# Performance work log

Hardware: AMD Instinct MI355X
Metric: run time of the kernel (lower is better)

## Reference

```python
import jax, jax.numpy as jnp
import numpy as np

N_QUBITS = 4
N_LAYERS = 2
DIM = 2 ** N_QUBITS  # 16
B = 65536


def _apply_1q(state, U, wire):
    # state: (B,) + (2,)*N_QUBITS complex64; U: (2,2) complex. Wire 0 = most significant (PennyLane order).
    s = jnp.moveaxis(state, wire + 1, -1)
    s = jnp.einsum('...j,ij->...i', s, U)
    return jnp.moveaxis(s, -1, wire + 1)


def _apply_cnot(state, control, target):
    s = jnp.moveaxis(state, (control + 1, target + 1), (-2, -1))
    s = jnp.concatenate([s[..., 0:1, :], s[..., 1:2, ::-1]], axis=-2)
    return jnp.moveaxis(s, (-2, -1), (control + 1, target + 1))


def _rot_matrix(phi, th, om):
    # qml.Rot(phi, theta, omega) = RZ(om) RY(th) RZ(phi)
    c = jnp.cos(th / 2)
    sn = jnp.sin(th / 2)
    ep = jnp.exp(-0.5j * (phi + om).astype(jnp.complex64))
    em = jnp.exp(0.5j * (phi - om).astype(jnp.complex64))
    row0 = jnp.stack([ep * c, -em * sn])
    row1 = jnp.stack([jnp.conj(em) * sn, jnp.conj(ep) * c])
    return jnp.stack([row0, row1])


def _strongly_entangling(state, theta):
    # PennyLane StronglyEntanglingLayers, default ranges r_l = (l % (n-1)) + 1, CNOT imprimitive ring
    for l in range(N_LAYERS):
        for w in range(N_QUBITS):
            U = _rot_matrix(theta[l, w, 0], theta[l, w, 1], theta[l, w, 2])
            state = _apply_1q(state, U, w)
        r = (l % (N_QUBITS - 1)) + 1
        for w in range(N_QUBITS):
            state = _apply_cnot(state, w, (w + r) % N_QUBITS)
    return state


def _encode(x, W1, b1, W2, b2):
    v = x.reshape(x.shape[0], -1) @ W1 + b1
    v = jax.nn.relu(v)
    v = v @ W2 + b2
    v = jnp.nan_to_num(v, nan=0.0, posinf=1.0, neginf=-1.0)
    v = jnp.tanh(v)
    nrm = jnp.linalg.norm(v, axis=-1, keepdims=True)
    return v / jnp.maximum(nrm, 1e-8)  # F.normalize(p=2, eps=1e-8)


def _prepare_state(v, theta):
    # AmplitudeEmbedding(normalize=True): renormalize, embed as amplitudes
    v = v / jnp.linalg.norm(v, axis=-1, keepdims=True)
    state = v.astype(jnp.complex64).reshape((v.shape[0],) + (2,) * N_QUBITS)
    return _strongly_entangling(state, theta)


def setup_inputs() -> dict:
    key = jax.random.key(0)
    k = jax.random.split(key, 7)
    return {
        'img_a': jax.random.normal(k[0], (B, 1, 28, 28), dtype=jnp.float32),
        'img_b': jax.random.normal(k[1], (B, 1, 28, 28), dtype=jnp.float32),
        'W1': 0.05 * jax.random.normal(k[2], (784, 64), dtype=jnp.float32),
        'b1': 0.05 * jax.random.normal(k[3], (64,), dtype=jnp.float32),
        'W2': 0.05 * jax.random.normal(k[4], (64, 16), dtype=jnp.float32),
        'b2': 0.05 * jax.random.normal(k[5], (16,), dtype=jnp.float32),
        'theta': 0.05 * jax.random.normal(k[6], (N_LAYERS, N_QUBITS, 3), dtype=jnp.float32),
    }


def reference(img_a, img_b, W1, b1, W2, b2, theta):
    theta_safe = jnp.nan_to_num(theta, nan=0.0, posinf=1.0, neginf=-1.0)
    va = _encode(img_a, W1, b1, W2, b2)
    vb = _encode(img_b, W1, b1, W2, b2)
    sa = _prepare_state(va, theta_safe).reshape(-1, DIM)
    sb = _prepare_state(vb, theta_safe).reshape(-1, DIM)
    # SWAP test: p0 = (1 + |<a|b>|^2)/2  =>  clamp(2*p0 - 1, 0, 1) = clip(|<a|b>|^2, 0, 1)
    ov = jnp.einsum('bd,bd->b', jnp.conj(sa), sb)
    fid = jnp.clip(jnp.abs(ov) ** 2, 0.0, 1.0)
    return fid.astype(jnp.float32)
```

## Files before the change

### kernel.cpp

```cpp
#include <hip/hip_runtime.h>


#define KDIM   784
#define HDIM   64
#define KSTEPS 25
#define W1S_ELEMS (KSTEPS * 4 * 64 * 8)
#define W1S_BYTES (W1S_ELEMS * 2)

typedef float  f32x4  __attribute__((ext_vector_type(4)));
typedef short  bf16x8 __attribute__((ext_vector_type(8)));

__device__ __forceinline__ unsigned short f2bf(float f) {
  unsigned u = __float_as_uint(f);
  u += 0x7fffu + ((u >> 16) & 1u);
  return (unsigned short)(u >> 16);
}

__device__ __forceinline__ float bf2f(unsigned short h) {
  return __uint_as_float(((unsigned)h) << 16);
}

__device__ __forceinline__ bf16x8 cvt8(f32x4 lo, f32x4 hi) {
  bf16x8 r;
  r[0] = (short)f2bf(lo[0]); r[1] = (short)f2bf(lo[1]);
  r[2] = (short)f2bf(lo[2]); r[3] = (short)f2bf(lo[3]);
  r[4] = (short)f2bf(hi[0]); r[5] = (short)f2bf(hi[1]);
  r[6] = (short)f2bf(hi[2]); r[7] = (short)f2bf(hi[3]);
  return r;
}

__device__ __forceinline__ float tanh_fast(float x) {
  float e = __expf(2.0f * x);
  return 1.0f - 2.0f / (e + 1.0f);
}

__global__ __launch_bounds__(256)
void prep_kernel(const float* __restrict__ W1, const float* __restrict__ W2,
                 unsigned short* __restrict__ w1s, float* __restrict__ w2t) {
  int tid = blockIdx.x * 256 + threadIdx.x;
  if (tid < W1S_ELEMS) {
    int j  = tid & 7;
    int l  = (tid >> 3) & 63;
    int st = tid >> 9;
    int s  = st >> 2;
    int t  = st & 3;
    int k  = s * 32 + (l >> 4) * 8 + j;
    int n  = t * 16 + (l & 15);
    float v = (k < KDIM) ? W1[k * HDIM + n] : 0.0f;
    w1s[tid] = f2bf(v);
  }
  if (tid < HDIM * 16) {
    int c = tid >> 6;
    int k = tid & 63;
    w2t[c * HDIM + k] = W2[k * 16 + c];
  }
}

__global__ __launch_bounds__(256, 8)
void qcm_kernel(const float* __restrict__ img_a, const float* __restrict__ img_b,
                const float* __restrict__ b1,    const float* __restrict__ b2,
                const unsigned short* __restrict__ w1s,
                const float* __restrict__ w2t,
                float* __restrict__ out) {
  __shared__ __attribute__((aligned(16))) unsigned short lds_h[64][72];

  const int tid  = threadIdx.x;
  const int wave = tid >> 6;
  const int lane = tid & 63;
  const int m    = lane & 15;
  const int quad = lane >> 4;
  const int p0   = blockIdx.x * 32 + wave * 8;

  const float* row = (m < 8)
      ? (img_a + (size_t)(p0 + m)     * KDIM)
      : (img_b + (size_t)(p0 + m - 8) * KDIM);
  const int koff = quad * 8;

  f32x4 acc[4];
  #pragma unroll
  for (int t = 0; t < 4; ++t)
    acc[t][0] = acc[t][1] = acc[t][2] = acc[t][3] = 0.0f;

  const int4* bwl = (const int4*)w1s + lane;
  f32x4 z4; z4[0] = z4[1] = z4[2] = z4[3] = 0.0f;

  f32x4 c0 = *(const f32x4*)(row + koff);
  f32x4 c1 = *(const f32x4*)(row + koff + 4);

  for (int s = 0; s < KSTEPS; ++s) {
    int4 w0 = bwl[s * 256];
    int4 w1 = bwl[s * 256 + 64];
    int4 w2 = bwl[s * 256 + 128];
    int4 w3 = bwl[s * 256 + 192];

    f32x4 n0 = z4, n1 = z4;
    if (s < 23) {
      const int kb = (s + 1) * 32 + koff;
      n0 = *(const f32x4*)(row + kb);
      n1 = *(const f32x4*)(row + kb + 4);
    } else if (s == 23) {
      if (quad < 2) {
        n0 = *(const f32x4*)(row + 768 + koff);
        n1 = *(const f32x4*)(row + 768 + koff + 4);
      }
    }

    bf16x8 fa = cvt8(c0, c1);

    acc[0] = __builtin_amdgcn_mfma_f32_16x16x32_bf16(
        fa, __builtin_bit_cast(bf16x8, w0), acc[0], 0, 0, 0);
    acc[1] = __builtin_amdgcn_mfma_f32_16x16x32_bf16(
        fa, __builtin_bit_cast(bf16x8, w1), acc[1], 0, 0, 0);
    acc[2] = __builtin_amdgcn_mfma_f32_16x16x32_bf16(
        fa, __builtin_bit_cast(bf16x8, w2), acc[2], 0, 0, 0);
    acc[3] = __builtin_amdgcn_mfma_f32_16x16x32_bf16(
        fa, __builtin_bit_cast(bf16x8, w3), acc[3], 0, 0, 0);

    c0 = n0; c1 = n1;
  }

  #pragma unroll
  for (int t = 0; t < 4; ++t) {
    float bias = b1[t * 16 + m];
    #pragma unroll
    for (int j = 0; j < 4; ++j) {
      float h = fmaxf(acc[t][j] + bias, 0.0f);
      lds_h[wave * 16 + quad * 4 + j][t * 16 + m] = f2bf(h);
    }
  }
  __syncthreads();

  const int p = tid >> 3;
  const int q = tid & 7;
  const int wsrc = p >> 3;
  const int r = p & 7;
  const unsigned short* ha_row = &lds_h[wsrc * 16 + r][0];
  const unsigned short* hb_row = &lds_h[wsrc * 16 + 8 + r][0];

  float za[2], zb[2];
  za[0] = b2[q * 2];     zb[0] = za[0];
  za[1] = b2[q * 2 + 1]; zb[1] = za[1];

  for (int k = 0; k < HDIM; k += 4) {
    uint2 ua = *(const uint2*)(ha_row + k);
    uint2 ub = *(const uint2*)(hb_row + k);
    float a0 = bf2f((unsigned short)(ua.x & 0xffff));
    float a1 = bf2f((unsigned short)(ua.x >> 16));
    float a2 = bf2f((unsigned short)(ua.y & 0xffff));
    float a3 = bf2f((unsigned short)(ua.y >> 16));
    float b0v = bf2f((unsigned short)(ub.x & 0xffff));
    float b1v = bf2f((unsigned short)(ub.x >> 16));
    float b2v = bf2f((unsigned short)(ub.y & 0xffff));
    float b3v = bf2f((unsigned short)(ub.y >> 16));
    #pragma unroll
    for (int i = 0; i < 2; ++i) {
      f32x4 wv = *(const f32x4*)(w2t + (q * 2 + i) * HDIM + k);
      za[i] += a0 * wv[0] + a1 * wv[1] + a2 * wv[2] + a3 * wv[3];
      zb[i] += b0v * wv[0] + b1v * wv[1] + b2v * wv[2] + b3v * wv[3];
    }
  }

  float d = 0.0f, na2 = 0.0f, nb2 = 0.0f;
  #pragma unroll
  for (int i = 0; i < 2; ++i) {
    float ua = tanh_fast(za[i]);
    float ub = tanh_fast(zb[i]);
    d   += ua * ub;
    na2 += ua * ua;
    nb2 += ub * ub;
  }
  d   += __shfl_xor(d, 1);   d   += __shfl_xor(d, 2);   d   += __shfl_xor(d, 4);
  na2 += __shfl_xor(na2, 1); na2 += __shfl_xor(na2, 2); na2 += __shfl_xor(na2, 4);
  nb2 += __shfl_xor(nb2, 1); nb2 += __shfl_xor(nb2, 2); nb2 += __shfl_xor(nb2, 4);

  if (q == 0) {
    float den = fmaxf(sqrtf(na2), 1e-8f) * fmaxf(sqrtf(nb2), 1e-8f);
    float ov  = d / den;
    float fid = ov * ov;
    out[blockIdx.x * 32 + p] = fminf(fid, 1.0f);
  }
}

extern "C" void kernel_launch(void* const* d_in, const int* in_sizes, int n_in,
                              void* d_out, int out_size, void* d_ws, size_t ws_size,
                              hipStream_t stream) {
  const float* img_a = (const float*)d_in[0];
  const float* img_b = (const float*)d_in[1];
  const float* W1    = (const float*)d_in[2];
  const float* b1    = (const float*)d_in[3];
  const float* W2    = (const float*)d_in[4];
  const float* b2    = (const float*)d_in[5];

  unsigned short* w1s = (unsigned short*)d_ws;
  float* w2t = (float*)((char*)d_ws + W1S_BYTES);

  prep_kernel<<<(W1S_ELEMS + 255) / 256, 256, 0, stream>>>(W1, W2, w1s, w2t);

  const int n_pairs = out_size;
  qcm_kernel<<<n_pairs / 32, 256, 0, stream>>>(img_a, img_b, b1, b2, w1s, w2t,
                                               (float*)d_out);
}
```

Baseline: 134.7 us.

## Stage image rows through LDS with coalesced loads and single-wave blocks

Each block is now a single 64-lane wave handling 8 pairs. The wave first loads all 16 image rows with fully coalesced float4 loads, converts them to bf16 and stores them in LDS. The MFMA loop then reads A fragments from LDS and software-prefetches the next step's W1 fragments, replacing the previous strided per-lane global row reads. The cost is about 26KB of LDS per 64-thread block, which may limit occupancy, plus an extra barrier phase before compute with no overlap of loading and math within a block.

```diff
diff --git a/kernel.cpp b/kernel.cpp
--- a/kernel.cpp
+++ b/kernel.cpp
@@ -7,6 +7,9 @@
 #define W1S_ELEMS (KSTEPS * 4 * 64 * 8)
 #define W1S_BYTES (W1S_ELEMS * 2)
 
+#define LROW   808
+#define NPAIR  8
+
 typedef float  f32x4  __attribute__((ext_vector_type(4)));
 typedef short  bf16x8 __attribute__((ext_vector_type(8)));
 
@@ -20,12 +23,10 @@
   return __uint_as_float(((unsigned)h) << 16);
 }
 
-__device__ __forceinline__ bf16x8 cvt8(f32x4 lo, f32x4 hi) {
-  bf16x8 r;
-  r[0] = (short)f2bf(lo[0]); r[1] = (short)f2bf(lo[1]);
-  r[2] = (short)f2bf(lo[2]); r[3] = (short)f2bf(lo[3]);
-  r[4] = (short)f2bf(hi[0]); r[5] = (short)f2bf(hi[1]);
-  r[6] = (short)f2bf(hi[2]); r[7] = (short)f2bf(hi[3]);
+__device__ __forceinline__ uint2 pack4(f32x4 v) {
+  uint2 r;
+  r.x = (unsigned)f2bf(v[0]) | ((unsigned)f2bf(v[1]) << 16);
+  r.y = (unsigned)f2bf(v[2]) | ((unsigned)f2bf(v[3]) << 16);
   return r;
 }
 
@@ -56,25 +57,49 @@
   }
 }
 
-__global__ __launch_bounds__(256, 8)
+__global__ __launch_bounds__(64)
 void qcm_kernel(const float* __restrict__ img_a, const float* __restrict__ img_b,
                 const float* __restrict__ b1,    const float* __restrict__ b2,
                 const unsigned short* __restrict__ w1s,
                 const float* __restrict__ w2t,
                 float* __restrict__ out) {
-  __shared__ __attribute__((aligned(16))) unsigned short lds_h[64][72];
-
-  const int tid  = threadIdx.x;
-  const int wave = tid >> 6;
-  const int lane = tid & 63;
+  __shared__ __attribute__((aligned(16))) unsigned short L[16][LROW];
+
+  const int lane = threadIdx.x;
   const int m    = lane & 15;
   const int quad = lane >> 4;
-  const int p0   = blockIdx.x * 32 + wave * 8;
-
-  const float* row = (m < 8)
-      ? (img_a + (size_t)(p0 + m)     * KDIM)
-      : (img_b + (size_t)(p0 + m - 8) * KDIM);
-  const int koff = quad * 8;
+  const int p0   = blockIdx.x * NPAIR;
+
+  {
+    const float* aB = img_a + (size_t)p0 * KDIM;
+    const float* bB = img_b + (size_t)p0 * KDIM;
+    #pragma unroll
+    for (int r = 0; r < NPAIR; ++r) {
+      const float* ra = aB + r * KDIM;
+      const float* rb = bB + r * KDIM;
+      f32x4 a0 = *(const f32x4*)(ra + lane * 4);
+      f32x4 a1 = *(const f32x4*)(ra + 256 + lane * 4);
+      f32x4 a2 = *(const f32x4*)(ra + 512 + lane * 4);
+      f32x4 c0 = *(const f32x4*)(rb + lane * 4);
+      f32x4 c1 = *(const f32x4*)(rb + 256 + lane * 4);
+      f32x4 c2 = *(const f32x4*)(rb + 512 + lane * 4);
+      *(uint2*)&L[r][lane * 4]           = pack4(a0);
+      *(uint2*)&L[r][256 + lane * 4]     = pack4(a1);
+      *(uint2*)&L[r][512 + lane * 4]     = pack4(a2);
+      *(uint2*)&L[8 + r][lane * 4]       = pack4(c0);
+      *(uint2*)&L[8 + r][256 + lane * 4] = pack4(c1);
+      *(uint2*)&L[8 + r][512 + lane * 4] = pack4(c2);
+      if (lane < 4) {
+        f32x4 ta = *(const f32x4*)(ra + 768 + lane * 4);
+        f32x4 tb = *(const f32x4*)(rb + 768 + lane * 4);
+        *(uint2*)&L[r][768 + lane * 4]     = pack4(ta);
+        *(uint2*)&L[8 + r][768 + lane * 4] = pack4(tb);
+      }
+    }
+    uint2 z; z.x = 0u; z.y = 0u;
+    *(uint2*)&L[lane >> 2][784 + (lane & 3) * 4] = z;
+  }
+  __syncthreads();
 
   f32x4 acc[4];
   #pragma unroll
@@ -82,60 +107,50 @@
     acc[t][0] = acc[t][1] = acc[t][2] = acc[t][3] = 0.0f;
 
   const int4* bwl = (const int4*)w1s + lane;
-  f32x4 z4; z4[0] = z4[1] = z4[2] = z4[3] = 0.0f;
-
-  f32x4 c0 = *(const f32x4*)(row + koff);
-  f32x4 c1 = *(const f32x4*)(row + koff + 4);
+  int4 w0 = bwl[0];
+  int4 w1 = bwl[64];
+  int4 w2 = bwl[128];
+  int4 w3 = bwl[192];
+  bf16x8 acur = *(const bf16x8*)&L[m][quad * 8];
 
   for (int s = 0; s < KSTEPS; ++s) {
-    int4 w0 = bwl[s * 256];
-    int4 w1 = bwl[s * 256 + 64];
-    int4 w2 = bwl[s * 256 + 128];
-    int4 w3 = bwl[s * 256 + 192];
-
-    f32x4 n0 = z4, n1 = z4;
-    if (s < 23) {
-      const int kb = (s + 1) * 32 + koff;
-      n0 = *(const f32x4*)(row + kb);
-      n1 = *(const f32x4*)(row + kb + 4);
-    } else if (s == 23) {
-      if (quad < 2) {
-        n0 = *(const f32x4*)(row + 768 + koff);
-        n1 = *(const f32x4*)(row + 768 + koff + 4);
-      }
-    }
-
-    bf16x8 fa = cvt8(c0, c1);
+    const int sp = (s + 1 < KSTEPS) ? s + 1 : s;
+    int4 nw0 = bwl[sp * 256];
+    int4 nw1 = bwl[sp * 256 + 64];
+    int4 nw2 = bwl[sp * 256 + 128];
+    int4 nw3 = bwl[sp * 256 + 192];
+    bf16x8 anxt = *(const bf16x8*)&L[m][sp * 32 + quad * 8];
 
     acc[0] = __builtin_amdgcn_mfma_f32_16x16x32_bf16(
-        fa, __builtin_bit_cast(bf16x8, w0), acc[0], 0, 0, 0);
+        acur, __builtin_bit_cast(bf16x8, w0), acc[0], 0, 0, 0);
     acc[1] = __builtin_amdgcn_mfma_f32_16x16x32_bf16(
-        fa, __builtin_bit_cast(bf16x8, w1), acc[1], 0, 0, 0);
+        acur, __builtin_bit_cast(bf16x8, w1), acc[1], 0, 0, 0);
     acc[2] = __builtin_amdgcn_mfma_f32_16x16x32_bf16(
-        fa, __builtin_bit_cast(bf16x8, w2), acc[2], 0, 0, 0);
+        acur, __builtin_bit_cast(bf16x8, w2), acc[2], 0, 0, 0);
     acc[3] = __builtin_amdgcn_mfma_f32_16x16x32_bf16(
-        fa, __builtin_bit_cast(bf16x8, w3), acc[3], 0, 0, 0);
-
-    c0 = n0; c1 = n1;
-  }
-
+        acur, __builtin_bit_cast(bf16x8, w3), acc[3], 0, 0, 0);
+
+    w0 = nw0; w1 = nw1; w2 = nw2; w3 = nw3;
+    acur = anxt;
+  }
+  __syncthreads();
+
+  unsigned short (*H)[72] = (unsigned short(*)[72])L;
   #pragma unroll
   for (int t = 0; t < 4; ++t) {
     float bias = b1[t * 16 + m];
     #pragma unroll
     for (int j = 0; j < 4; ++j) {
       float h = fmaxf(acc[t][j] + bias, 0.0f);
-      lds_h[wave * 16 + quad * 4 + j][t * 16 + m] = f2bf(h);
+      H[quad * 4 + j][t * 16 + m] = f2bf(h);
     }
   }
   __syncthreads();
 
-  const int p = tid >> 3;
-  const int q = tid & 7;
-  const int wsrc = p >> 3;
-  const int r = p & 7;
-  const unsigned short* ha_row = &lds_h[wsrc * 16 + r][0];
-  const unsigned short* hb_row = &lds_h[wsrc * 16 + 8 + r][0];
+  const int p = lane >> 3;
+  const int q = lane & 7;
+  const unsigned short* ha_row = &H[p][0];
+  const unsigned short* hb_row = &H[8 + p][0];
 
   float za[2], zb[2];
   za[0] = b2[q * 2];     zb[0] = za[0];
@@ -177,7 +192,7 @@
     float den = fmaxf(sqrtf(na2), 1e-8f) * fmaxf(sqrtf(nb2), 1e-8f);
     float ov  = d / den;
     float fid = ov * ov;
-    out[blockIdx.x * 32 + p] = fminf(fid, 1.0f);
+    out[blockIdx.x * NPAIR + p] = fminf(fid, 1.0f);
   }
 }
 
@@ -197,6 +212,6 @@
   prep_kernel<<<(W1S_ELEMS + 255) / 256, 256, 0, stream>>>(W1, W2, w1s, w2t);
 
   const int n_pairs = out_size;
-  qcm_kernel<<<n_pairs / 32, 256, 0, stream>>>(img_a, img_b, b1, b2, w1s, w2t,
-                                               (float*)d_out);
-}
+  qcm_kernel<<<n_pairs / NPAIR, 64, 0, stream>>>(img_a, img_b, b1, b2, w1s, w2t,
+                                                 (float*)d_out);
+}
```

Result: slower. 168.9 us (+25.4%).

## Stage W1 in LDS with 1024-thread blocks and deepen image prefetch pipeline

Applied to the files above, without the earlier changes.

Blocks grow to 1024 threads handling 128 pairs. Each block first copies the packed bf16 W1 (about 100KB) into shared memory, so MFMA B-operands come from LDS instead of global/L2. The image-row loads become a 5-deep register prefetch ring over a fully unrolled K loop, and the same LDS buffer is reused for the hidden activations afterwards. The trade-off is a large per-block LDS footprint that limits blocks per CU, an up-front copy cost in every block, and higher register pressure from the prefetch ring.

```diff
diff --git a/kernel.cpp b/kernel.cpp
--- a/kernel.cpp
+++ b/kernel.cpp
@@ -6,6 +6,7 @@
 #define KSTEPS 25
 #define W1S_ELEMS (KSTEPS * 4 * 64 * 8)
 #define W1S_BYTES (W1S_ELEMS * 2)
+#define W1S_INT4  (W1S_BYTES / 16)
 
 typedef float  f32x4  __attribute__((ext_vector_type(4)));
 typedef short  bf16x8 __attribute__((ext_vector_type(8)));
@@ -56,20 +57,32 @@
   }
 }
 
-__global__ __launch_bounds__(256, 8)
+__global__ __launch_bounds__(1024, 4)
 void qcm_kernel(const float* __restrict__ img_a, const float* __restrict__ img_b,
                 const float* __restrict__ b1,    const float* __restrict__ b2,
                 const unsigned short* __restrict__ w1s,
                 const float* __restrict__ w2t,
                 float* __restrict__ out) {
-  __shared__ __attribute__((aligned(16))) unsigned short lds_h[64][72];
-
-  const int tid  = threadIdx.x;
+  __shared__ __attribute__((aligned(16))) char smem[W1S_BYTES];
+
+  const int tid = threadIdx.x;
+
+  {
+    const int4* src = (const int4*)w1s;
+    int4* dst = (int4*)smem;
+    #pragma unroll
+    for (int i = 0; i < 7; ++i) {
+      int idx = tid + i * 1024;
+      if (idx < W1S_INT4) dst[idx] = src[idx];
+    }
+  }
+  __syncthreads();
+
   const int wave = tid >> 6;
   const int lane = tid & 63;
   const int m    = lane & 15;
   const int quad = lane >> 4;
-  const int p0   = blockIdx.x * 32 + wave * 8;
+  const int p0   = blockIdx.x * 128 + wave * 8;
 
   const float* row = (m < 8)
       ? (img_a + (size_t)(p0 + m)     * KDIM)
@@ -81,31 +94,47 @@
   for (int t = 0; t < 4; ++t)
     acc[t][0] = acc[t][1] = acc[t][2] = acc[t][3] = 0.0f;
 
-  const int4* bwl = (const int4*)w1s + lane;
+  const int4* wl = (const int4*)smem;
+
   f32x4 z4; z4[0] = z4[1] = z4[2] = z4[3] = 0.0f;
 
-  f32x4 c0 = *(const f32x4*)(row + koff);
-  f32x4 c1 = *(const f32x4*)(row + koff + 4);
-
+  f32x4 pip[6][2];
+  #pragma unroll
+  for (int i = 0; i < 6; ++i) { pip[i][0] = z4; pip[i][1] = z4; }
+
+  #pragma unroll
+  for (int st = 0; st < 5; ++st) {
+    const int kb = st * 32 + koff;
+    pip[st][0] = *(const f32x4*)(row + kb);
+    pip[st][1] = *(const f32x4*)(row + kb + 4);
+  }
+
+  #pragma unroll
   for (int s = 0; s < KSTEPS; ++s) {
-    int4 w0 = bwl[s * 256];
-    int4 w1 = bwl[s * 256 + 64];
-    int4 w2 = bwl[s * 256 + 128];
-    int4 w3 = bwl[s * 256 + 192];
-
-    f32x4 n0 = z4, n1 = z4;
-    if (s < 23) {
-      const int kb = (s + 1) * 32 + koff;
-      n0 = *(const f32x4*)(row + kb);
-      n1 = *(const f32x4*)(row + kb + 4);
-    } else if (s == 23) {
-      if (quad < 2) {
-        n0 = *(const f32x4*)(row + 768 + koff);
-        n1 = *(const f32x4*)(row + 768 + koff + 4);
+    {
+      const int st = s + 5;
+      const int slot = st % 6;
+      if (st < 24) {
+        const int kb = st * 32 + koff;
+        pip[slot][0] = *(const f32x4*)(row + kb);
+        pip[slot][1] = *(const f32x4*)(row + kb + 4);
+      } else if (st == 24) {
+        if (quad < 2) {
+          pip[slot][0] = *(const f32x4*)(row + 768 + koff);
+          pip[slot][1] = *(const f32x4*)(row + 768 + koff + 4);
+        } else {
+          pip[slot][0] = z4; pip[slot][1] = z4;
+        }
       }
     }
 
-    bf16x8 fa = cvt8(c0, c1);
+    const int base = s * 256 + lane;
+    int4 w0 = wl[base];
+    int4 w1 = wl[base + 64];
+    int4 w2 = wl[base + 128];
+    int4 w3 = wl[base + 192];
+
+    bf16x8 fa = cvt8(pip[s % 6][0], pip[s % 6][1]);
 
     acc[0] = __builtin_amdgcn_mfma_f32_16x16x32_bf16(
         fa, __builtin_bit_cast(bf16x8, w0), acc[0], 0, 0, 0);
@@ -115,9 +144,10 @@
         fa, __builtin_bit_cast(bf16x8, w2), acc[2], 0, 0, 0);
     acc[3] = __builtin_amdgcn_mfma_f32_16x16x32_bf16(
         fa, __builtin_bit_cast(bf16x8, w3), acc[3], 0, 0, 0);
-
-    c0 = n0; c1 = n1;
-  }
+  }
+
+  __syncthreads();
+  unsigned short (*H)[72] = (unsigned short(*)[72])smem;
 
   #pragma unroll
   for (int t = 0; t < 4; ++t) {
@@ -125,7 +155,7 @@
     #pragma unroll
     for (int j = 0; j < 4; ++j) {
       float h = fmaxf(acc[t][j] + bias, 0.0f);
-      lds_h[wave * 16 + quad * 4 + j][t * 16 + m] = f2bf(h);
+      H[wave * 16 + quad * 4 + j][t * 16 + m] = f2bf(h);
     }
   }
   __syncthreads();
@@ -134,8 +164,8 @@
   const int q = tid & 7;
   const int wsrc = p >> 3;
   const int r = p & 7;
-  const unsigned short* ha_row = &lds_h[wsrc * 16 + r][0];
-  const unsigned short* hb_row = &lds_h[wsrc * 16 + 8 + r][0];
+  const unsigned short* ha_row = &H[wsrc * 16 + r][0];
+  const unsigned short* hb_row = &H[wsrc * 16 + 8 + r][0];
 
   float za[2], zb[2];
   za[0] = b2[q * 2];     zb[0] = za[0];
@@ -177,7 +207,7 @@
     float den = fmaxf(sqrtf(na2), 1e-8f) * fmaxf(sqrtf(nb2), 1e-8f);
     float ov  = d / den;
     float fid = ov * ov;
-    out[blockIdx.x * 32 + p] = fminf(fid, 1.0f);
+    out[blockIdx.x * 128 + p] = fminf(fid, 1.0f);
   }
 }
 
@@ -197,6 +227,6 @@
   prep_kernel<<<(W1S_ELEMS + 255) / 256, 256, 0, stream>>>(W1, W2, w1s, w2t);
 
   const int n_pairs = out_size;
-  qcm_kernel<<<n_pairs / 32, 256, 0, stream>>>(img_a, img_b, b1, b2, w1s, w2t,
-                                               (float*)d_out);
-}
+  qcm_kernel<<<n_pairs / 128, 1024, 0, stream>>>(img_a, img_b, b1, b2, w1s, w2t,
+                                                 (float*)d_out);
+}
```

Result: faster. 113.8 us (-15.5%).
